# Kernel tuning notes

Measured on AMD Instinct MI355X. Metric: run time of the kernel, lower is better.

## Reference

```python
import jax, jax.numpy as jnp
import numpy as np

N_NODES = 100000


def setup_inputs() -> dict:
    key = jax.random.key(0)
    k1, k2, k3, k4, k5, k6 = jax.random.split(key, 6)
    x = jax.random.normal(k1, (N_NODES, 6), dtype=jnp.float32)
    edge_index = jax.random.randint(k2, (2, 6400000), 0, N_NODES, dtype=jnp.int64)
    # PointCloudGNN.lin: Linear(6, 64); PointCloudModel.lin: Linear(64, 3)
    W1 = jax.random.normal(k3, (64, 6), dtype=jnp.float32) * (1.0 / np.sqrt(6))
    b1 = jax.random.normal(k4, (64,), dtype=jnp.float32) * 0.01
    W2 = jax.random.normal(k5, (3, 64), dtype=jnp.float32) * (1.0 / np.sqrt(64))
    b2 = jax.random.normal(k6, (3,), dtype=jnp.float32) * 0.01
    return {"x": x, "edge_index": edge_index, "W1": W1, "b1": b1, "W2": W2, "b2": b2}


def reference(x, edge_index, W1, b1, W2, b2):
    n = x.shape[0]
    # add_self_loops: append (i, i) for every node
    loops = jnp.arange(n, dtype=edge_index.dtype)
    row = jnp.concatenate([edge_index[0], loops])  # source nodes (j)
    col = jnp.concatenate([edge_index[1], loops])  # target nodes (i)
    # linear transform: [N, 6] -> [N, 64]
    h = x @ W1.T + b1
    # degree computed over row (as in the source), self-loops guarantee deg >= 1
    deg = jax.ops.segment_sum(jnp.ones_like(row, dtype=h.dtype), row, num_segments=n)
    deg_inv_sqrt = deg ** -0.5
    norm = deg_inv_sqrt[row] * deg_inv_sqrt[col]  # [E+N]
    # message: norm * x_j (x_j = h[row]); aggregate (add) at col
    msg = norm[:, None] * h[row]  # [E+N, 64]
    agg = jax.ops.segment_sum(msg, col, num_segments=n)  # [N, 64]
    out = jax.nn.relu(agg) @ W2.T + b2  # [N, 3]
    return out
```

## Files before the change

kernel.cpp:

```cpp
#include <hip/hip_runtime.h>

#define NTHREADS 256
#define SD     128
#define NMAX   102400
#define BAGG   256
#define APAD   9
#define LBITS  8
#define SA     2
#define MAXBIN 512
#define CHUNK  8192

#define QSCALE 2097152.0f
#define QINV   (1.0f / 2097152.0f)
#define FSCALE 4096.0f
#define FINV   (1.0f / 4096.0f)

__global__ __launch_bounds__(1024)
void k_deg(const int* __restrict__ row, int E, int n,
           unsigned char* __restrict__ degPart) {
    __shared__ unsigned int h[NMAX / 4];
    for (int i = threadIdx.x; i < NMAX / 4; i += blockDim.x) h[i] = 0u;
    __syncthreads();

    const int s = blockIdx.x;
    const int E4 = E >> 2;
    const int c4 = (E4 + SD - 1) / SD;
    const int s4 = s * c4;
    const int e4 = min(s4 + c4, E4);
    const int4* row4 = (const int4*)row;
    for (int t = s4 + threadIdx.x; t < e4; t += blockDim.x) {
        int4 r = row4[t];
        atomicAdd(&h[r.x >> 2], 1u << ((r.x & 3) << 3));
        atomicAdd(&h[r.y >> 2], 1u << ((r.y & 3) << 3));
        atomicAdd(&h[r.z >> 2], 1u << ((r.z & 3) << 3));
        atomicAdd(&h[r.w >> 2], 1u << ((r.w & 3) << 3));
    }
    if (s == SD - 1 && threadIdx.x == 0) {
        for (int e = E & ~3; e < E; ++e) {
            int v = row[e];
            atomicAdd(&h[v >> 2], 1u << ((v & 3) << 3));
        }
    }
    __syncthreads();

    unsigned int* gp = (unsigned int*)degPart;
    const int nw = n >> 2;
    for (int i = threadIdx.x; i < nw; i += blockDim.x)
        gp[(size_t)s * nw + i] = h[i];
}

__global__ void k_disy(const unsigned char* __restrict__ degPart,
                       const float* __restrict__ x, int n,
                       float* __restrict__ dis, int* __restrict__ yq) {
    const int nw = n >> 2;
    int p = blockIdx.x * blockDim.x + threadIdx.x;
    if (p >= nw) return;
    const unsigned int* gp = (const unsigned int*)degPart;
    unsigned s0 = 0, s1 = 0, s2 = 0, s3 = 0;
    for (int s = 0; s < SD; ++s) {
        unsigned w = gp[(size_t)s * nw + p];
        s0 += w & 255u;
        s1 += (w >> 8) & 255u;
        s2 += (w >> 16) & 255u;
        s3 += w >> 24;
    }
    unsigned ss[4] = {s0, s1, s2, s3};
    const float2* x2 = (const float2*)x;
    const int i0 = p * 4;
    #pragma unroll
    for (int k = 0; k < 4; ++k) {
        int i = i0 + k;
        float d = rsqrtf((float)ss[k] + 1.0f);
        dis[i] = d;
        float2 a = x2[3 * i + 0], b = x2[3 * i + 1], c = x2[3 * i + 2];
        float fs = d * FSCALE;
        float vals[6] = {fs * a.x, fs * a.y, fs * b.x, fs * b.y, fs * c.x, fs * c.y};
        int q[6];
        #pragma unroll
        for (int m = 0; m < 6; ++m)
            q[m] = __float2int_rn(fminf(fmaxf(vals[m], -32767.0f), 32767.0f));
        int4* q4 = (int4*)(yq + (size_t)i * 4);
        q4[0] = make_int4((q[0] & 0xffff) | (q[1] << 16),
                          (q[2] & 0xffff) | (q[3] << 16),
                          (q[4] & 0xffff) | (q[5] << 16),
                          __float2int_rn(d * QSCALE));
    }
}

__global__ __launch_bounds__(1024)
void k_bin(const int* __restrict__ col, const int* __restrict__ row,
           int E, int cap, unsigned int* __restrict__ bins,
           int* __restrict__ binCursor) {
    __shared__ int cnt[MAXBIN];
    __shared__ int cnt2[MAXBIN];
    __shared__ int base[MAXBIN];
    for (int i = threadIdx.x; i < MAXBIN; i += blockDim.x) { cnt[i] = 0; cnt2[i] = 0; }
    __syncthreads();

    const int E4 = E >> 2;
    const int s4 = blockIdx.x * (CHUNK / 4);
    const int e4 = min(s4 + CHUNK / 4, E4);
    const bool last = (e4 == E4);
    const int4* col4 = (const int4*)col;
    const int4* row4 = (const int4*)row;

    for (int t = s4 + threadIdx.x; t < e4; t += blockDim.x) {
        int4 c = col4[t];
        atomicAdd(&cnt[c.x >> LBITS], 1);
        atomicAdd(&cnt[c.y >> LBITS], 1);
        atomicAdd(&cnt[c.z >> LBITS], 1);
        atomicAdd(&cnt[c.w >> LBITS], 1);
    }
    if (last && threadIdx.x == 0)
        for (int e = E & ~3; e < E; ++e) atomicAdd(&cnt[col[e] >> LBITS], 1);
    __syncthreads();

    if (threadIdx.x < MAXBIN && cnt[threadIdx.x] > 0)
        base[threadIdx.x] = atomicAdd(&binCursor[threadIdx.x], cnt[threadIdx.x]);
    __syncthreads();

    for (int t = s4 + threadIdx.x; t < e4; t += blockDim.x) {
        int4 c = col4[t];
        int4 r = row4[t];
        int b, p, idx;
        b = c.x >> LBITS; p = atomicAdd(&cnt2[b], 1); idx = base[b] + p;
        if (idx < cap) bins[(size_t)b * cap + idx] = (unsigned)(c.x & (BAGG - 1)) | ((unsigned)r.x << LBITS);
        b = c.y >> LBITS; p = atomicAdd(&cnt2[b], 1); idx = base[b] + p;
        if (idx < cap) bins[(size_t)b * cap + idx] = (unsigned)(c.y & (BAGG - 1)) | ((unsigned)r.y << LBITS);
        b = c.z >> LBITS; p = atomicAdd(&cnt2[b], 1); idx = base[b] + p;
        if (idx < cap) bins[(size_t)b * cap + idx] = (unsigned)(c.z & (BAGG - 1)) | ((unsigned)r.z << LBITS);
        b = c.w >> LBITS; p = atomicAdd(&cnt2[b], 1); idx = base[b] + p;
        if (idx < cap) bins[(size_t)b * cap + idx] = (unsigned)(c.w & (BAGG - 1)) | ((unsigned)r.w << LBITS);
    }
    if (last && threadIdx.x == 0) {
        for (int e = E & ~3; e < E; ++e) {
            int b = col[e] >> LBITS;
            int p = atomicAdd(&cnt2[b], 1);
            int idx = base[b] + p;
            if (idx < cap)
                bins[(size_t)b * cap + idx] = (unsigned)(col[e] & (BAGG - 1)) | ((unsigned)row[e] << LBITS);
        }
    }
}

__global__ __launch_bounds__(256)
void k_agg2(const unsigned int* __restrict__ bins, const int* __restrict__ binCursor,
            const int* __restrict__ yq, float* __restrict__ aggPart,
            int n, int cap) {
    __shared__ int acc[BAGG * APAD];
    const int b = blockIdx.x / SA;
    const int s = blockIdx.x % SA;
    const int lo = b * BAGG;

    for (int i = threadIdx.x; i < BAGG * APAD; i += blockDim.x) acc[i] = 0;
    __syncthreads();

    int cnt = binCursor[b];
    if (cnt > cap) cnt = cap;
    const int chunk = (((cnt + SA - 1) / SA) + 3) & ~3;
    const int st = min(s * chunk, cnt);
    const int en = min(st + chunk, cnt);
    const int len = en - st;
    const int len4 = len >> 2;
    const unsigned int* bp = bins + (size_t)b * cap;
    const uint4* bp4 = (const uint4*)(bp + st);
    const int4* y4 = (const int4*)yq;

    #define ACCUM(lv, pk)                                                  \
        {                                                                  \
            int* qq = acc + (lv) * APAD;                                   \
            atomicAdd(qq + 0, (int)(short)((pk).x & 0xffff));              \
            atomicAdd(qq + 1, (pk).x >> 16);                               \
            atomicAdd(qq + 2, (int)(short)((pk).y & 0xffff));              \
            atomicAdd(qq + 3, (pk).y >> 16);                               \
            atomicAdd(qq + 4, (int)(short)((pk).z & 0xffff));              \
            atomicAdd(qq + 5, (pk).z >> 16);                               \
            atomicAdd(qq + 6, (pk).w);                                     \
        }

    for (int q = threadIdx.x; q < len4; q += blockDim.x) {
        uint4 v = bp4[q];
        unsigned l0 = v.x & (BAGG - 1u); int j0 = (int)(v.x >> LBITS);
        unsigned l1 = v.y & (BAGG - 1u); int j1 = (int)(v.y >> LBITS);
        unsigned l2 = v.z & (BAGG - 1u); int j2 = (int)(v.z >> LBITS);
        unsigned l3 = v.w & (BAGG - 1u); int j3 = (int)(v.w >> LBITS);
        int4 p0 = y4[j0];
        int4 p1 = y4[j1];
        int4 p2 = y4[j2];
        int4 p3 = y4[j3];
        ACCUM(l0, p0)
        ACCUM(l1, p1)
        ACCUM(l2, p2)
        ACCUM(l3, p3)
    }
    for (int t = st + len4 * 4 + threadIdx.x; t < en; t += blockDim.x) {
        unsigned v = bp[t];
        unsigned l = v & (BAGG - 1u);
        int j = (int)(v >> LBITS);
        int4 pk = y4[j];
        ACCUM(l, pk)
    }
    #undef ACCUM
    __syncthreads();

    const int nb = min(BAGG, n - lo);
    for (int i = threadIdx.x; i < nb; i += blockDim.x) {
        const int* src = acc + (size_t)i * APAD;
        float4* op = (float4*)(aggPart + ((size_t)s * n + (lo + i)) * 8);
        op[0] = make_float4((float)src[0] * FINV, (float)src[1] * FINV,
                            (float)src[2] * FINV, (float)src[3] * FINV);
        op[1] = make_float4((float)src[4] * FINV, (float)src[5] * FINV,
                            (float)src[6] * QINV, 0.0f);
    }
}

__global__ void k_final_r(const float* __restrict__ x, const float* __restrict__ dis,
                          const float* __restrict__ aggPart,
                          const float* __restrict__ W1, const float* __restrict__ b1,
                          const float* __restrict__ W2, const float* __restrict__ b2,
                          float* __restrict__ out, int n) {
    __shared__ float sW1[64 * 6];
    __shared__ float sb1[64];
    __shared__ float sW2[3 * 64];
    __shared__ float sb2[3];
    for (int k = threadIdx.x; k < 64 * 6; k += blockDim.x) sW1[k] = W1[k];
    for (int k = threadIdx.x; k < 64; k += blockDim.x) sb1[k] = b1[k];
    for (int k = threadIdx.x; k < 3 * 64; k += blockDim.x) sW2[k] = W2[k];
    if (threadIdx.x < 3) sb2[threadIdx.x] = b2[threadIdx.x];
    __syncthreads();

    int i = blockIdx.x * blockDim.x + threadIdx.x;
    if (i >= n) return;

    float4 G0 = make_float4(0.f, 0.f, 0.f, 0.f);
    float4 G1 = make_float4(0.f, 0.f, 0.f, 0.f);
    for (int s = 0; s < SA; ++s) {
        const float4* pp = (const float4*)(aggPart + ((size_t)s * n + i) * 8);
        float4 a = pp[0], b = pp[1];
        G0.x += a.x; G0.y += a.y; G0.z += a.z; G0.w += a.w;
        G1.x += b.x; G1.y += b.y; G1.z += b.z;
    }

    float di = dis[i];
    const float2* x2 = (const float2*)x;
    float2 xa = x2[3 * i + 0], xb = x2[3 * i + 1], xc = x2[3 * i + 2];

    float ax[6];
    ax[0] = di * (G0.x + di * xa.x);
    ax[1] = di * (G0.y + di * xa.y);
    ax[2] = di * (G0.z + di * xb.x);
    ax[3] = di * (G0.w + di * xb.y);
    ax[4] = di * (G1.x + di * xc.x);
    ax[5] = di * (G1.y + di * xc.y);
    float s = di * (G1.z + di);

    float o0 = sb2[0], o1 = sb2[1], o2 = sb2[2];
    for (int f = 0; f < 64; ++f) {
        float v = s * sb1[f];
        #pragma unroll
        for (int k = 0; k < 6; ++k) v = fmaf(ax[k], sW1[f * 6 + k], v);
        v = fmaxf(v, 0.0f);
        o0 = fmaf(v, sW2[0 * 64 + f], o0);
        o1 = fmaf(v, sW2[1 * 64 + f], o1);
        o2 = fmaf(v, sW2[2 * 64 + f], o2);
    }
    out[(size_t)i * 3 + 0] = o0;
    out[(size_t)i * 3 + 1] = o1;
    out[(size_t)i * 3 + 2] = o2;
}

__global__ void k_count1(const int* __restrict__ idx, int E, int* __restrict__ cnt) {
    int t = blockIdx.x * blockDim.x + threadIdx.x;
    int e = t * 4;
    if (e + 3 < E) {
        int4 r = ((const int4*)idx)[t];
        atomicAdd(&cnt[r.x], 1); atomicAdd(&cnt[r.y], 1);
        atomicAdd(&cnt[r.z], 1); atomicAdd(&cnt[r.w], 1);
    } else if (e < E) {
        for (int q = e; q < E; ++q) atomicAdd(&cnt[idx[q]], 1);
    }
}
__global__ void k_dis(const int* __restrict__ cnt, float* __restrict__ dis, int n) {
    int t = blockIdx.x * blockDim.x + threadIdx.x;
    if (t < n) dis[t] = rsqrtf((float)cnt[t] + 1.0f);
}
__global__ void k_scatter(const int* __restrict__ row, const int* __restrict__ col,
                          const float* __restrict__ x, const float* __restrict__ dis,
                          float* __restrict__ agg, int E) {
    int e = blockIdx.x * blockDim.x + threadIdx.x;
    if (e >= E) return;
    int j = row[e];
    int i = col[e];
    float w = dis[j];
    const float2* x2 = (const float2*)x;
    float2 a = x2[3 * j + 0], b = x2[3 * j + 1], c = x2[3 * j + 2];
    float* p = agg + (size_t)i * 8;
    atomicAdd(p + 0, w * a.x); atomicAdd(p + 1, w * a.y);
    atomicAdd(p + 2, w * b.x); atomicAdd(p + 3, w * b.y);
    atomicAdd(p + 4, w * c.x); atomicAdd(p + 5, w * c.y);
    atomicAdd(p + 6, w);
}
__global__ void k_final(const float* __restrict__ x, const float* __restrict__ dis,
                        const float* __restrict__ agg,
                        const float* __restrict__ W1, const float* __restrict__ b1,
                        const float* __restrict__ W2, const float* __restrict__ b2,
                        float* __restrict__ out, int n) {
    __shared__ float sW1[64 * 6];
    __shared__ float sb1[64];
    __shared__ float sW2[3 * 64];
    __shared__ float sb2[3];
    for (int k = threadIdx.x; k < 64 * 6; k += blockDim.x) sW1[k] = W1[k];
    for (int k = threadIdx.x; k < 64; k += blockDim.x) sb1[k] = b1[k];
    for (int k = threadIdx.x; k < 3 * 64; k += blockDim.x) sW2[k] = W2[k];
    if (threadIdx.x < 3) sb2[threadIdx.x] = b2[threadIdx.x];
    __syncthreads();
    int i = blockIdx.x * blockDim.x + threadIdx.x;
    if (i >= n) return;
    float di = dis[i];
    const float4* ag4 = (const float4*)(agg + (size_t)i * 8);
    float4 g0 = ag4[0], g1 = ag4[1];
    const float2* x2 = (const float2*)x;
    float2 xa = x2[3 * i + 0], xb = x2[3 * i + 1], xc = x2[3 * i + 2];
    float ax[6];
    ax[0] = di * (g0.x + di * xa.x);
    ax[1] = di * (g0.y + di * xa.y);
    ax[2] = di * (g0.z + di * xb.x);
    ax[3] = di * (g0.w + di * xb.y);
    ax[4] = di * (g1.x + di * xc.x);
    ax[5] = di * (g1.y + di * xc.y);
    float s = di * (g1.z + di);
    float o0 = sb2[0], o1 = sb2[1], o2 = sb2[2];
    for (int f = 0; f < 64; ++f) {
        float v = s * sb1[f];
        #pragma unroll
        for (int k = 0; k < 6; ++k) v = fmaf(ax[k], sW1[f * 6 + k], v);
        v = fmaxf(v, 0.0f);
        o0 = fmaf(v, sW2[0 * 64 + f], o0);
        o1 = fmaf(v, sW2[1 * 64 + f], o1);
        o2 = fmaf(v, sW2[2 * 64 + f], o2);
    }
    out[(size_t)i * 3 + 0] = o0;
    out[(size_t)i * 3 + 1] = o1;
    out[(size_t)i * 3 + 2] = o2;
}

extern "C" void kernel_launch(void* const* d_in, const int* in_sizes, int n_in,
                              void* d_out, int out_size, void* d_ws, size_t ws_size,
                              hipStream_t stream) {
    const float* x  = (const float*)d_in[0];
    const int*   ei = (const int*)d_in[1];
    const float* W1 = (const float*)d_in[2];
    const float* b1 = (const float*)d_in[3];
    const float* W2 = (const float*)d_in[4];
    const float* b2 = (const float*)d_in[5];
    float* out = (float*)d_out;

    const int n = in_sizes[0] / 6;
    const int E = in_sizes[1] / 2;
    const int* row = ei;
    const int* col = ei + E;

    auto align1k = [](size_t v) { return (v + 1023) & ~(size_t)1023; };

    const int nbin = (n + BAGG - 1) / BAGG;
    const int cap  = ((E / nbin) + 1024 + 3) & ~3;

    size_t curOff  = 0;
    size_t regAOff = align1k(curOff + MAXBIN * 4);
    size_t regABytes = (size_t)SD * n;
    size_t binsBytes = (size_t)nbin * cap * 4;
    if (binsBytes > regABytes) regABytes = binsBytes;
    size_t aggOff  = align1k(regAOff + regABytes);
    size_t yOff    = align1k(aggOff + (size_t)SA * n * 8 * 4);
    size_t disOff  = align1k(yOff + (size_t)n * 4 * 4);
    size_t needed  = disOff + (size_t)n * 4;

    char* ws = (char*)d_ws;
    const bool okMain = ((E & 3) == 0) && ((n & 3) == 0) && (n <= NMAX) &&
                        (n <= (1 << 17)) && (nbin <= MAXBIN) && (ws_size >= needed);

    if (okMain) {
        int* binCursor            = (int*)(ws + curOff);
        unsigned char* degPart    = (unsigned char*)(ws + regAOff);
        unsigned int* bins        = (unsigned int*)(ws + regAOff);
        float* aggPart            = (float*)(ws + aggOff);
        int*   yq                 = (int*)(ws + yOff);
        float* dis                = (float*)(ws + disOff);

        hipMemsetAsync(binCursor, 0, MAXBIN * 4, stream);

        k_deg<<<SD, 1024, 0, stream>>>(row, E, n, degPart);

        int nw = n >> 2;
        k_disy<<<(nw + NTHREADS - 1) / NTHREADS, NTHREADS, 0, stream>>>(degPart, x, n, dis, yq);

        int nbBlocks = (E + CHUNK - 1) / CHUNK;
        k_bin<<<nbBlocks, 1024, 0, stream>>>(col, row, E, cap, bins, binCursor);

        k_agg2<<<nbin * SA, 256, 0, stream>>>(bins, binCursor, yq, aggPart, n, cap);

        int blocksN = (n + NTHREADS - 1) / NTHREADS;
        k_final_r<<<blocksN, NTHREADS, 0, stream>>>(x, dis, aggPart, W1, b1, W2, b2, out, n);
    } else {
        size_t fDisOff = align1k((size_t)n * 4);
        size_t fAggOff = align1k(fDisOff + (size_t)n * 4);
        int*   fCnt = (int*)ws;
        float* fDis = (float*)(ws + fDisOff);
        float* fAgg = (float*)(ws + fAggOff);

        hipMemsetAsync(ws, 0, fAggOff + (size_t)n * 8 * 4, stream);
        int threads4 = (E + 3) / 4;
        int blocksE4 = (threads4 + NTHREADS - 1) / NTHREADS;
        int blocksN  = (n + NTHREADS - 1) / NTHREADS;
        k_count1<<<blocksE4, NTHREADS, 0, stream>>>(row, E, fCnt);
        k_dis<<<blocksN, NTHREADS, 0, stream>>>(fCnt, fDis, n);
        int blocksE = (E + NTHREADS - 1) / NTHREADS;
        k_scatter<<<blocksE, NTHREADS, 0, stream>>>(row, col, x, fDis, fAgg, E);
        k_final<<<blocksN, NTHREADS, 0, stream>>>(x, fDis, fAgg, W1, b1, W2, b2, out, n);
    }
}
```

Measured before the change: 127.3 us.

## Stage binned edges in shared memory for coalesced bin writes

The binning kernel now prefix-sums the per-chunk bin counts in shared memory and scatters each edge into a local shared buffer sorted by bin. It then writes the buffer out in order, so consecutive threads store to contiguous global addresses within each bin instead of scattering. This targets uncoalesced global writes, at the cost of about 48KB of LDS per block, extra barriers and a scan. The tail handling for E not divisible by 4 was removed, which drops edges if E%4 != 0. E is 6.4M here, so no edges are lost.

```diff
diff --git a/kernel.cpp b/kernel.cpp
--- a/kernel.cpp
+++ b/kernel.cpp
@@ -92,15 +92,18 @@
            int E, int cap, unsigned int* __restrict__ bins,
            int* __restrict__ binCursor) {
     __shared__ int cnt[MAXBIN];
-    __shared__ int cnt2[MAXBIN];
+    __shared__ int lofs[MAXBIN];
     __shared__ int base[MAXBIN];
-    for (int i = threadIdx.x; i < MAXBIN; i += blockDim.x) { cnt[i] = 0; cnt2[i] = 0; }
+    __shared__ int cur[MAXBIN];
+    __shared__ unsigned int ent[CHUNK];
+    __shared__ unsigned short ebin[CHUNK];
+
+    for (int i = threadIdx.x; i < MAXBIN; i += blockDim.x) { cnt[i] = 0; cur[i] = 0; }
     __syncthreads();
 
     const int E4 = E >> 2;
     const int s4 = blockIdx.x * (CHUNK / 4);
     const int e4 = min(s4 + CHUNK / 4, E4);
-    const bool last = (e4 == E4);
     const int4* col4 = (const int4*)col;
     const int4* row4 = (const int4*)row;
 
@@ -111,35 +114,48 @@
         atomicAdd(&cnt[c.z >> LBITS], 1);
         atomicAdd(&cnt[c.w >> LBITS], 1);
     }
-    if (last && threadIdx.x == 0)
-        for (int e = E & ~3; e < E; ++e) atomicAdd(&cnt[col[e] >> LBITS], 1);
-    __syncthreads();
-
-    if (threadIdx.x < MAXBIN && cnt[threadIdx.x] > 0)
-        base[threadIdx.x] = atomicAdd(&binCursor[threadIdx.x], cnt[threadIdx.x]);
+    __syncthreads();
+
+    if (threadIdx.x < MAXBIN) lofs[threadIdx.x] = cnt[threadIdx.x];
+    __syncthreads();
+    for (int d = 1; d < MAXBIN; d <<= 1) {
+        int v = 0;
+        if (threadIdx.x >= d && threadIdx.x < MAXBIN) v = lofs[threadIdx.x - d];
+        __syncthreads();
+        if (threadIdx.x >= d && threadIdx.x < MAXBIN) lofs[threadIdx.x] += v;
+        __syncthreads();
+    }
+    if (threadIdx.x < MAXBIN) {
+        lofs[threadIdx.x] -= cnt[threadIdx.x];
+        if (cnt[threadIdx.x] > 0)
+            base[threadIdx.x] = atomicAdd(&binCursor[threadIdx.x], cnt[threadIdx.x]);
+    }
     __syncthreads();
 
     for (int t = s4 + threadIdx.x; t < e4; t += blockDim.x) {
         int4 c = col4[t];
         int4 r = row4[t];
-        int b, p, idx;
-        b = c.x >> LBITS; p = atomicAdd(&cnt2[b], 1); idx = base[b] + p;
-        if (idx < cap) bins[(size_t)b * cap + idx] = (unsigned)(c.x & (BAGG - 1)) | ((unsigned)r.x << LBITS);
-        b = c.y >> LBITS; p = atomicAdd(&cnt2[b], 1); idx = base[b] + p;
-        if (idx < cap) bins[(size_t)b * cap + idx] = (unsigned)(c.y & (BAGG - 1)) | ((unsigned)r.y << LBITS);
-        b = c.z >> LBITS; p = atomicAdd(&cnt2[b], 1); idx = base[b] + p;
-        if (idx < cap) bins[(size_t)b * cap + idx] = (unsigned)(c.z & (BAGG - 1)) | ((unsigned)r.z << LBITS);
-        b = c.w >> LBITS; p = atomicAdd(&cnt2[b], 1); idx = base[b] + p;
-        if (idx < cap) bins[(size_t)b * cap + idx] = (unsigned)(c.w & (BAGG - 1)) | ((unsigned)r.w << LBITS);
-    }
-    if (last && threadIdx.x == 0) {
-        for (int e = E & ~3; e < E; ++e) {
-            int b = col[e] >> LBITS;
-            int p = atomicAdd(&cnt2[b], 1);
-            int idx = base[b] + p;
-            if (idx < cap)
-                bins[(size_t)b * cap + idx] = (unsigned)(col[e] & (BAGG - 1)) | ((unsigned)row[e] << LBITS);
-        }
+        int b, p;
+        b = c.x >> LBITS; p = lofs[b] + atomicAdd(&cur[b], 1);
+        ent[p] = (unsigned)(c.x & (BAGG - 1)) | ((unsigned)r.x << LBITS);
+        ebin[p] = (unsigned short)b;
+        b = c.y >> LBITS; p = lofs[b] + atomicAdd(&cur[b], 1);
+        ent[p] = (unsigned)(c.y & (BAGG - 1)) | ((unsigned)r.y << LBITS);
+        ebin[p] = (unsigned short)b;
+        b = c.z >> LBITS; p = lofs[b] + atomicAdd(&cur[b], 1);
+        ent[p] = (unsigned)(c.z & (BAGG - 1)) | ((unsigned)r.z << LBITS);
+        ebin[p] = (unsigned short)b;
+        b = c.w >> LBITS; p = lofs[b] + atomicAdd(&cur[b], 1);
+        ent[p] = (unsigned)(c.w & (BAGG - 1)) | ((unsigned)r.w << LBITS);
+        ebin[p] = (unsigned short)b;
+    }
+    __syncthreads();
+
+    const int total = (e4 - s4) * 4;
+    for (int i = threadIdx.x; i < total; i += blockDim.x) {
+        int b = ebin[i];
+        int dst = base[b] + (i - lofs[b]);
+        if (dst < cap) bins[(size_t)b * cap + dst] = ent[i];
     }
 }
 
```

After: 109.0 us. -14.4%, faster.
